# Kernel optimization log

Measured on AMD Instinct MI355X. Metric: run time of the kernel, lower is better.

The kernel has to match this reference:

```python
import jax, jax.numpy as jnp
import numpy as np

BAND = 15  # band_part(0, 15): keep 0 <= j - i <= 15


def setup_inputs() -> dict:
    key = jax.random.key(0)
    k1, k2 = jax.random.split(key)
    B, L = 8, 4096
    s = jax.random.normal(k1, (B, L), dtype=jnp.float32)
    e = jax.random.normal(k2, (B, L), dtype=jnp.float32)
    return {"s": s, "e": e}


def reference(s, e):
    # outer[b, i, j] = s[b, i] * e[b, j], masked to upper band of width 16
    L = s.shape[1]
    i = jnp.arange(L)[:, None]
    j = jnp.arange(L)[None, :]
    band_mask = (j >= i) & (j - i <= BAND)  # [L, L] bool
    outer = s[:, :, None] * e[:, None, :]   # [B, L, L]
    return jnp.where(band_mask[None], outer, jnp.zeros((), dtype=outer.dtype))
```

## Files before the change

kernel.cpp:

```cpp
#include <hip/hip_runtime.h>


#define BAND 15
#define LDIM 4096
#define CHUNKS 16

typedef float f32x4 __attribute__((ext_vector_type(4)));

__global__ __launch_bounds__(256) void band_outer_rows(
    const float* __restrict__ s,
    const float* __restrict__ e,
    float* __restrict__ out) {
  const int wave = threadIdx.x >> 6;
  const int lane = threadIdx.x & 63;
  const int row  = (blockIdx.x << 2) + wave;
  const int i    = row & (LDIM - 1);
  const int b    = row >> 12;

  const float sv = s[row];
  const float* __restrict__ eb = e + (b << 12);
  f32x4* __restrict__ out4 =
      reinterpret_cast<f32x4*>(out) + (size_t)row * (LDIM / 4) + lane;

  const int c_lo = i >> 8;
  const int c_hi = (i + BAND) >> 8;

  const f32x4 z = {0.f, 0.f, 0.f, 0.f};
#pragma unroll
  for (int c = 0; c < CHUNKS; ++c) {
    if (c == c_lo || c == c_hi) {
      const int j0 = (c << 8) + (lane << 2);
      f32x4 v;
#pragma unroll
      for (int k = 0; k < 4; ++k) {
        const int j = j0 + k;
        v[k] = (j >= i && j - i <= BAND) ? sv * eb[j] : 0.f;
      }
      out4[c * 64] = v;
    } else {
      out4[c * 64] = z;
    }
  }
}

extern "C" void kernel_launch(void* const* d_in, const int* in_sizes, int n_in,
                              void* d_out, int out_size, void* d_ws, size_t ws_size,
                              hipStream_t stream) {
  const float* s = (const float*)d_in[0];
  const float* e = (const float*)d_in[1];
  float* out = (float*)d_out;

  const int rows = out_size / LDIM;
  band_outer_rows<<<rows / 4, 256, 0, stream>>>(s, e, out);
}
```

Before: 101.7 us.

## Split into grid-stride zero fill plus sparse band patch kernel

Replaces the single fused per-row writer with two launches: a grid-stride kernel that zeroes the whole output with vector stores, then a one-thread-per-row kernel that writes the 16 band entries. This simplifies the main store loop and drops the per-chunk branching. The band region is written twice, and the patch kernel issues strided scalar stores with poor coalescing. It also adds a second launch and a dependency between the two kernels.

```diff
diff --git a/kernel.cpp b/kernel.cpp
--- a/kernel.cpp
+++ b/kernel.cpp
@@ -3,44 +3,32 @@
 
 #define BAND 15
 #define LDIM 4096
-#define CHUNKS 16
 
 typedef float f32x4 __attribute__((ext_vector_type(4)));
 
-__global__ __launch_bounds__(256) void band_outer_rows(
+__global__ __launch_bounds__(256) void zero_fill(f32x4* __restrict__ out,
+                                                 int n4) {
+  int idx = blockIdx.x * blockDim.x + threadIdx.x;
+  int stride = gridDim.x * blockDim.x;
+  const f32x4 z = {0.f, 0.f, 0.f, 0.f};
+  for (int t = idx; t < n4; t += stride) out[t] = z;
+}
+
+__global__ __launch_bounds__(256) void band_patch(
     const float* __restrict__ s,
     const float* __restrict__ e,
     float* __restrict__ out) {
-  const int wave = threadIdx.x >> 6;
-  const int lane = threadIdx.x & 63;
-  const int row  = (blockIdx.x << 2) + wave;
-  const int i    = row & (LDIM - 1);
-  const int b    = row >> 12;
+  const int tid = blockIdx.x * blockDim.x + threadIdx.x;
+  const int i = tid & (LDIM - 1);
+  const int b = tid >> 12;
 
-  const float sv = s[row];
+  const float sv = s[tid];
   const float* __restrict__ eb = e + (b << 12);
-  f32x4* __restrict__ out4 =
-      reinterpret_cast<f32x4*>(out) + (size_t)row * (LDIM / 4) + lane;
+  float* __restrict__ orow = out + (size_t)tid * LDIM;
 
-  const int c_lo = i >> 8;
-  const int c_hi = (i + BAND) >> 8;
-
-  const f32x4 z = {0.f, 0.f, 0.f, 0.f};
-#pragma unroll
-  for (int c = 0; c < CHUNKS; ++c) {
-    if (c == c_lo || c == c_hi) {
-      const int j0 = (c << 8) + (lane << 2);
-      f32x4 v;
-#pragma unroll
-      for (int k = 0; k < 4; ++k) {
-        const int j = j0 + k;
-        v[k] = (j >= i && j - i <= BAND) ? sv * eb[j] : 0.f;
-      }
-      out4[c * 64] = v;
-    } else {
-      out4[c * 64] = z;
-    }
-  }
+  const int jmax = min(i + BAND, LDIM - 1);
+#pragma unroll 4
+  for (int j = i; j <= jmax; ++j) orow[j] = sv * eb[j];
 }
 
 extern "C" void kernel_launch(void* const* d_in, const int* in_sizes, int n_in,
@@ -50,6 +38,9 @@
   const float* e = (const float*)d_in[1];
   float* out = (float*)d_out;
 
+  const int n4 = out_size / 4;
+  zero_fill<<<2048, 256, 0, stream>>>(reinterpret_cast<f32x4*>(out), n4);
+
   const int rows = out_size / LDIM;
-  band_outer_rows<<<rows / 4, 256, 0, stream>>>(s, e, out);
+  band_patch<<<rows / 256, 256, 0, stream>>>(s, e, out);
 }
```

Result: slower. 134.9 us (+32.6%).
